# Kernel optimization log

Hardware: AMD Instinct MI355X
Metric: run time of the kernel (lower is better)

Reference implementation:

```python
import jax, jax.numpy as jnp
import numpy as np

H = 100
EPS = 1e-5


def _ln(x, g, b):
    m = jnp.mean(x, axis=-1, keepdims=True)
    v = jnp.mean((x - m) ** 2, axis=-1, keepdims=True)
    return (x - m) / jnp.sqrt(v + EPS) * g + b


def _enc(x, W, b, g, be):
    # Linear -> Tanh -> LayerNorm
    return _ln(jnp.tanh(x @ W + b), g, be)


def setup_inputs() -> dict:
    key = jax.random.key(0)
    ks = jax.random.split(key, 16)
    B, N = 32768, 16
    obs_dim = 4 + 3 * N + 2 * (N - 1) + 2 * N  # 114
    d = {
        'inputs': jax.random.normal(ks[0], (B, obs_dim), dtype=jnp.float32),
        'agent_num': N,
        'sW': jax.random.normal(ks[1], (4, H), dtype=jnp.float32) * 0.5,
        'sb': jnp.zeros((H,), jnp.float32),
        'sg': jnp.ones((H,), jnp.float32),
        'sbe': jnp.zeros((H,), jnp.float32),
        'oW': jax.random.normal(ks[2], (2, H), dtype=jnp.float32) * 0.5,
        'ob': jnp.zeros((H,), jnp.float32),
        'og': jnp.ones((H,), jnp.float32),
        'obe': jnp.zeros((H,), jnp.float32),
        'lW': jax.random.normal(ks[3], (3, H), dtype=jnp.float32) * 0.5,
        'lb': jnp.zeros((H,), jnp.float32),
        'lg': jnp.ones((H,), jnp.float32),
        'lbe': jnp.zeros((H,), jnp.float32),
        'gW': jax.random.normal(ks[4], (2, H), dtype=jnp.float32) * 0.5,
        'gb': jnp.zeros((H,), jnp.float32),
        'gg': jnp.ones((H,), jnp.float32),
        'gbe': jnp.zeros((H,), jnp.float32),
        'Ac': jax.random.normal(ks[5], (H, H), dtype=jnp.float32) * 0.1,
        'Lc': jax.random.normal(ks[6], (H, H), dtype=jnp.float32) * 0.1,
        'fcW': jax.random.normal(ks[7], (H, H), dtype=jnp.float32) * 0.1,
        'fcb': jnp.zeros((H,), jnp.float32),
        'fcg': jnp.ones((H,), jnp.float32),
        'fcbe': jnp.zeros((H,), jnp.float32),
        'f1W': jax.random.normal(ks[8], (4 * H, H), dtype=jnp.float32) * 0.05,
        'f1b': jnp.zeros((H,), jnp.float32),
        'f1g': jnp.ones((H,), jnp.float32),
        'f1be': jnp.zeros((H,), jnp.float32),
        'f2W': jax.random.normal(ks[9], (H, H), dtype=jnp.float32) * 0.1,
        'f2b': jnp.zeros((H,), jnp.float32),
        'f2g': jnp.ones((H,), jnp.float32),
        'f2be': jnp.zeros((H,), jnp.float32),
    }
    return d


def reference(inputs, agent_num, sW, sb, sg, sbe, oW, ob, og, obe, lW, lb, lg, lbe, gW, gb, gg, gbe, Ac, Lc, fcW, fcb, fcg, fcbe, f1W, f1b, f1g, f1be, f2W, f2b, f2g, f2be):
    N = agent_num
    B = inputs.shape[0]
    self_emb = _enc(inputs[:, :4], sW, sb, sg, sbe)  # [B,H]
    lm = inputs[:, 4:4 + 3 * N].reshape(B, N, 3)
    off = 4 + 3 * N
    oth = inputs[:, off:off + 2 * (N - 1)].reshape(B, N - 1, 2)
    off2 = off + 2 * (N - 1)
    gl = inputs[:, off2:off2 + 2 * N].reshape(B, N, 2)
    oth_e = _enc(oth, oW, ob, og, obe)    # [B,N-1,H]
    lm_e = _enc(lm, lW, lb, lg, lbe)      # [B,N,H]
    gl_e = _enc(gl, gW, gb, gg, gbe)      # [B,N,H]
    qa = self_emb @ Ac                    # [B,H]
    ql = self_emb @ Lc                    # [B,H] (also used for goal: bug preserved from source)
    alpha_a = jax.nn.softmax(jnp.einsum('bh,bnh->bn', qa, oth_e), axis=1)
    va = jnp.einsum('bn,bnh->bh', alpha_a, oth_e)
    alpha_l = jax.nn.softmax(jnp.einsum('bh,bnh->bn', ql, lm_e), axis=1)
    vl = jnp.einsum('bn,bnh->bh', alpha_l, lm_e)
    alpha_g = jax.nn.softmax(jnp.einsum('bh,bnh->bn', ql, gl_e), axis=1)
    vg = jnp.einsum('bn,bnh->bh', alpha_g, gl_e)
    gi = _enc(self_emb, fcW, fcb, fcg, fcbe)
    x = jnp.concatenate([gi, va, vl, vg], axis=1)  # [B,4H]
    h = _enc(x, f1W, f1b, f1g, f1be)
    return _enc(h, f2W, f2b, f2g, f2be)
```

## Files before the change

kernel.cpp:

```cpp
#include <hip/hip_runtime.h>
#include <math.h>

#define OBS 114
#define ROWS_PER_BLOCK 16
#define BSTRIDE 104

__device__ __forceinline__ float fast_tanh(float x) {
    float e = __expf(2.0f * x);
    return 1.0f - 2.0f * __builtin_amdgcn_rcpf(e + 1.0f);
}

template<int CTRL>
__device__ __forceinline__ float dpp_add(float x) {
    int y = __builtin_amdgcn_update_dpp(0, __float_as_int(x), CTRL, 0xF, 0xF, true);
    return x + __int_as_float(y);
}
__device__ __forceinline__ float row16_sum(float x) {
    x = dpp_add<0xB1>(x);
    x = dpp_add<0x4E>(x);
    x = dpp_add<0x124>(x);
    x = dpp_add<0x128>(x);
    return x;
}
__device__ __forceinline__ float f4c(const float4& v, int j) {
    return j==0?v.x: j==1?v.y: j==2?v.z: v.w;
}

__global__ __launch_bounds__(256) void repack_kernel(
    const float* __restrict__ Ac, const float* __restrict__ Lc,
    const float* __restrict__ fcW, const float* __restrict__ f1W,
    const float* __restrict__ f2W, float* __restrict__ ws)
{
    int tid = blockIdx.x*256 + threadIdx.x;
    if (tid >= 800*128) return;
    int krow = tid >> 7;
    int idx  = tid & 127;
    int j = idx >> 3, i = idx & 7;
    int h = j + 16*i;
    const float* src; int k;
    if (krow < 100)      { src = Ac;  k = krow; }
    else if (krow < 200) { src = Lc;  k = krow-100; }
    else if (krow < 300) { src = fcW; k = krow-200; }
    else if (krow < 700) { src = f1W; k = krow-300; }
    else                 { src = f2W; k = krow-700; }
    float v = (i < 7 && h < 100) ? src[k*100 + h] : 0.f;
    ws[tid] = v;
}

template<int NK4>
__device__ __forceinline__ void mm16(const float* __restrict__ Wp,
    const float (*sbuf)[BSTRIDE], int R0, int R1, int j, float acc[7][2])
{
    const float* wp = Wp + j*8;
#pragma unroll 2
    for (int k4 = 0; k4 < NK4; ++k4) {
        float4 xa = *(const float4*)&sbuf[R0][k4*4];
        float4 xb = *(const float4*)&sbuf[R1][k4*4];
#pragma unroll
        for (int jj=0;jj<4;++jj) {
            const float* w8 = wp + (size_t)(k4*4+jj)*128;
            float4 wlo = *(const float4*)w8;
            float4 whi = *(const float4*)(w8+4);
            float w[7] = {wlo.x,wlo.y,wlo.z,wlo.w,whi.x,whi.y,whi.z};
            float xka = f4c(xa,jj), xkb = f4c(xb,jj);
#pragma unroll
            for (int i=0;i<7;++i) {
                acc[i][0] = fmaf(xka, w[i], acc[i][0]);
                acc[i][1] = fmaf(xkb, w[i], acc[i][1]);
            }
        }
    }
}

template<int K, int NA>
__device__ __forceinline__ void attn16(
    const float* __restrict__ W, const float* __restrict__ bb,
    const float* __restrict__ gp, const float* __restrict__ bep,
    const float* __restrict__ in, int xoff,
    float (*sbuf)[BSTRIDE],
    int rowAc, int rowBc, int RA, int RB,
    const float qacc[7][2],
    const int hc[7], const float msk[7])
{
    float w[K][7], bias[7], g[7], be[7];
#pragma unroll
    for (int i=0;i<7;++i) {
#pragma unroll
        for (int k=0;k<K;++k) w[k][i] = W[k*100 + hc[i]] * msk[i];
        bias[i] = bb[hc[i]] * msk[i];
        g[i]    = gp[hc[i]] * msk[i];
        be[i]   = bep[hc[i]];
    }
    float qg[2][7], C1[2];
#pragma unroll
    for (int b=0;b<2;++b) {
        float c = 0.f;
#pragma unroll
        for (int i=0;i<7;++i) { qg[b][i] = qacc[i][b]*g[i]; c += qg[b][i]; }
        C1[b] = row16_sum(c);
    }
    const float* xr0 = in + (size_t)rowAc*OBS + xoff;
    const float* xr1 = in + (size_t)rowBc*OBS + xoff;
    float s[2] = {0.f,0.f}, bacc[2] = {0.f,0.f};
    float A[2][7];
#pragma unroll
    for (int b=0;b<2;++b)
#pragma unroll
        for (int i=0;i<7;++i) A[b][i]=0.f;

#pragma unroll 1
    for (int n=0;n<NA;++n) {
        float x0[K], x1[K];
#pragma unroll
        for (int k=0;k<K;++k) { x0[k] = xr0[n*K+k]; x1[k] = xr1[n*K+k]; }
        float t[2][7], sa[2], sq[2], sd[2];
#pragma unroll
        for (int b=0;b<2;++b) { sa[b]=0.f; sq[b]=0.f; sd[b]=0.f; }
#pragma unroll
        for (int i=0;i<7;++i) {
#pragma unroll
            for (int b=0;b<2;++b) {
                float a = bias[i];
#pragma unroll
                for (int k=0;k<K;++k) a = fmaf(b ? x1[k] : x0[k], w[k][i], a);
                float tt = fast_tanh(a);
                t[b][i] = tt;
                sa[b] += tt;
                sq[b] = fmaf(tt,tt,sq[b]);
                sd[b] = fmaf(qg[b][i],tt,sd[b]);
            }
        }
#pragma unroll
        for (int b=0;b<2;++b) { sa[b]=row16_sum(sa[b]); sq[b]=row16_sum(sq[b]); sd[b]=row16_sum(sd[b]); }
#pragma unroll
        for (int b=0;b<2;++b) {
            float mean = sa[b]*0.01f;
            float var  = fmaf(sq[b],0.01f,-mean*mean);
            float rinv = __builtin_amdgcn_rsqf(var + 1e-5f);
            float logit = (sd[b]-mean*C1[b])*rinv;
            float wgt = __expf(fminf(logit,80.f));
            s[b] += wgt;
            float wr = wgt*rinv;
            bacc[b] = fmaf(wr,mean,bacc[b]);
#pragma unroll
            for (int i=0;i<7;++i) A[b][i] = fmaf(wr,t[b][i],A[b][i]);
        }
    }
#pragma unroll
    for (int b=0;b<2;++b) {
        int R = b ? RB : RA;
        float inv = __builtin_amdgcn_rcpf(s[b]);
#pragma unroll
        for (int i=0;i<7;++i)
            if (msk[i]>0.f) sbuf[R][hc[i]] = fmaf(g[i], (A[b][i]-bacc[b])*inv, be[i]);
    }
}

__device__ __forceinline__ void ln_pair(const float acc[7][2],
    const float* __restrict__ bp, const float* __restrict__ gp, const float* __restrict__ bep,
    const int hc[7], const float msk[7], float outv[2][7])
{
    float bias[7], g[7], be[7];
#pragma unroll
    for (int i=0;i<7;++i) { bias[i]=bp[hc[i]]*msk[i]; g[i]=gp[hc[i]]; be[i]=bep[hc[i]]; }
    float t[2][7], sa[2], sq[2];
#pragma unroll
    for (int b=0;b<2;++b) { sa[b]=0.f; sq[b]=0.f; }
#pragma unroll
    for (int i=0;i<7;++i) {
#pragma unroll
        for (int b=0;b<2;++b) {
            float tt = fast_tanh(acc[i][b] + bias[i]);
            t[b][i] = tt; sa[b] += tt*msk[i]; sq[b] = fmaf(tt*msk[i],tt,sq[b]);
        }
    }
#pragma unroll
    for (int b=0;b<2;++b) { sa[b]=row16_sum(sa[b]); sq[b]=row16_sum(sq[b]); }
#pragma unroll
    for (int b=0;b<2;++b) {
        float mean = sa[b]*0.01f;
        float var  = fmaf(sq[b],0.01f,-mean*mean);
        float rinv = __builtin_amdgcn_rsqf(var + 1e-5f);
#pragma unroll
        for (int i=0;i<7;++i) outv[b][i] = fmaf((t[b][i]-mean)*rinv, g[i], be[i]);
    }
}

__global__ __launch_bounds__(128, 4)
void obs_encoder_kernel(const float* __restrict__ in,
    const float* __restrict__ sW, const float* __restrict__ sb, const float* __restrict__ sg, const float* __restrict__ sbe,
    const float* __restrict__ oW, const float* __restrict__ ob, const float* __restrict__ og, const float* __restrict__ obe,
    const float* __restrict__ lW, const float* __restrict__ lb, const float* __restrict__ lg, const float* __restrict__ lbe,
    const float* __restrict__ gW, const float* __restrict__ gb, const float* __restrict__ gg_, const float* __restrict__ gbe,
    const float* __restrict__ fcb, const float* __restrict__ fcg, const float* __restrict__ fcbe,
    const float* __restrict__ f1b, const float* __restrict__ f1g, const float* __restrict__ f1be,
    const float* __restrict__ f2b, const float* __restrict__ f2g, const float* __restrict__ f2be,
    const float* __restrict__ wsf,
    float* __restrict__ out, int B)
{
    const int lane = threadIdx.x & 63;
    const int wv   = threadIdx.x >> 6;
    const int j    = lane & 15;
    const int rw   = lane >> 4;
    const int rowBase = blockIdx.x*ROWS_PER_BLOCK + wv*8;
    const int rowA = rowBase + rw;
    const int rowB = rowBase + 4 + rw;
    const int RA = wv*8 + rw, RB = RA + 4;
    const int rowAc = min(rowA, B-1), rowBc = min(rowB, B-1);

    int hc[7]; float msk[7];
#pragma unroll
    for (int i=0;i<7;++i) {
        int h = j + 16*i;
        bool v = h < 100;
        hc[i] = v ? h : 99;
        msk[i] = v ? 1.f : 0.f;
    }

    __shared__ __align__(16) float sbuf[ROWS_PER_BLOCK][BSTRIDE];

    const float* Acp = wsf;
    const float* Lcp = wsf + 12800;
    const float* fcp = wsf + 25600;
    const float* f1p = wsf + 38400;
    const float* f2p = wsf + 89600;

    {
        float w[4][7], bias[7], g[7], be[7];
#pragma unroll
        for (int i=0;i<7;++i) {
#pragma unroll
            for (int k=0;k<4;++k) w[k][i] = sW[k*100 + hc[i]] * msk[i];
            bias[i] = sb[hc[i]] * msk[i]; g[i] = sg[hc[i]]; be[i] = sbe[hc[i]];
        }
        const float* xr0 = in + (size_t)rowAc*OBS;
        const float* xr1 = in + (size_t)rowBc*OBS;
        float x[2][4];
#pragma unroll
        for (int k=0;k<4;++k) { x[0][k]=xr0[k]; x[1][k]=xr1[k]; }
        float t[2][7], sa[2], sq[2];
#pragma unroll
        for (int b=0;b<2;++b) { sa[b]=0.f; sq[b]=0.f; }
#pragma unroll
        for (int i=0;i<7;++i) {
#pragma unroll
            for (int b=0;b<2;++b) {
                float a = bias[i];
#pragma unroll
                for (int k=0;k<4;++k) a = fmaf(x[b][k], w[k][i], a);
                float tt = fast_tanh(a);
                t[b][i] = tt; sa[b] += tt*msk[i]; sq[b] = fmaf(tt*msk[i],tt,sq[b]);
            }
        }
#pragma unroll
        for (int b=0;b<2;++b) { sa[b]=row16_sum(sa[b]); sq[b]=row16_sum(sq[b]); }
#pragma unroll
        for (int b=0;b<2;++b) {
            int R = b ? RB : RA;
            float mean = sa[b]*0.01f;
            float var  = fmaf(sq[b],0.01f,-mean*mean);
            float rinv = __builtin_amdgcn_rsqf(var + 1e-5f);
#pragma unroll
            for (int i=0;i<7;++i)
                if (msk[i] > 0.f) sbuf[R][hc[i]] = fmaf((t[b][i]-mean)*rinv, g[i], be[i]);
        }
    }

    float accA[7][2], accL[7][2], accF[7][2];
#pragma unroll
    for (int i=0;i<7;++i) { accA[i][0]=accA[i][1]=accL[i][0]=accL[i][1]=accF[i][0]=accF[i][1]=0.f; }
    mm16<25>(Acp, sbuf, RA, RB, j, accA);
    mm16<25>(Lcp, sbuf, RA, RB, j, accL);
    mm16<25>(fcp, sbuf, RA, RB, j, accF);

    float f1a[7][2];
#pragma unroll
    for (int i=0;i<7;++i) { f1a[i][0]=0.f; f1a[i][1]=0.f; }

    {
        float outv[2][7];
        ln_pair(accF, fcb, fcg, fcbe, hc, msk, outv);
#pragma unroll
        for (int b=0;b<2;++b) {
            int R = b ? RB : RA;
#pragma unroll
            for (int i=0;i<7;++i)
                if (msk[i] > 0.f) sbuf[R][hc[i]] = outv[b][i];
        }
    }
    mm16<25>(f1p, sbuf, RA, RB, j, f1a);

    attn16<2,15>(oW, ob, og,  obe, in, 52, sbuf, rowAc, rowBc, RA, RB, accA, hc, msk);
    mm16<25>(f1p + 100*128, sbuf, RA, RB, j, f1a);
    attn16<3,16>(lW, lb, lg,  lbe, in, 4,  sbuf, rowAc, rowBc, RA, RB, accL, hc, msk);
    mm16<25>(f1p + 200*128, sbuf, RA, RB, j, f1a);
    attn16<2,16>(gW, gb, gg_, gbe, in, 82, sbuf, rowAc, rowBc, RA, RB, accL, hc, msk);
    mm16<25>(f1p + 300*128, sbuf, RA, RB, j, f1a);

    {
        float outv[2][7];
        ln_pair(f1a, f1b, f1g, f1be, hc, msk, outv);
#pragma unroll
        for (int b=0;b<2;++b) {
            int R = b ? RB : RA;
#pragma unroll
            for (int i=0;i<7;++i)
                if (msk[i] > 0.f) sbuf[R][hc[i]] = outv[b][i];
        }
    }

    {
        float acc[7][2];
#pragma unroll
        for (int i=0;i<7;++i) { acc[i][0]=0.f; acc[i][1]=0.f; }
        mm16<25>(f2p, sbuf, RA, RB, j, acc);
        float outv[2][7];
        ln_pair(acc, f2b, f2g, f2be, hc, msk, outv);
#pragma unroll
        for (int b=0;b<2;++b) {
            int row = b ? rowB : rowA;
            if (row < B) {
#pragma unroll
                for (int i=0;i<7;++i)
                    if (msk[i] > 0.f)
                        out[(size_t)row*100 + hc[i]] = outv[b][i];
            }
        }
    }
}

extern "C" void kernel_launch(void* const* d_in, const int* in_sizes, int n_in,
                              void* d_out, int out_size, void* d_ws, size_t ws_size,
                              hipStream_t stream) {
    const float* in  = (const float*)d_in[0];
    const float* sW  = (const float*)d_in[2];
    const float* sb  = (const float*)d_in[3];
    const float* sg  = (const float*)d_in[4];
    const float* sbe = (const float*)d_in[5];
    const float* oW  = (const float*)d_in[6];
    const float* ob  = (const float*)d_in[7];
    const float* og  = (const float*)d_in[8];
    const float* obe = (const float*)d_in[9];
    const float* lW  = (const float*)d_in[10];
    const float* lb  = (const float*)d_in[11];
    const float* lg  = (const float*)d_in[12];
    const float* lbe = (const float*)d_in[13];
    const float* gW  = (const float*)d_in[14];
    const float* gb  = (const float*)d_in[15];
    const float* gg  = (const float*)d_in[16];
    const float* gbe = (const float*)d_in[17];
    const float* Ac  = (const float*)d_in[18];
    const float* Lc  = (const float*)d_in[19];
    const float* fcW = (const float*)d_in[20];
    const float* fcb = (const float*)d_in[21];
    const float* fcg = (const float*)d_in[22];
    const float* fcbe= (const float*)d_in[23];
    const float* f1W = (const float*)d_in[24];
    const float* f1b = (const float*)d_in[25];
    const float* f1g = (const float*)d_in[26];
    const float* f1be= (const float*)d_in[27];
    const float* f2W = (const float*)d_in[28];
    const float* f2b = (const float*)d_in[29];
    const float* f2g = (const float*)d_in[30];
    const float* f2be= (const float*)d_in[31];
    float* out = (float*)d_out;
    float* wsf = (float*)d_ws;

    int B = in_sizes[0] / OBS;
    repack_kernel<<<(800*128 + 255)/256, 256, 0, stream>>>(Ac, Lc, fcW, f1W, f2W, wsf);
    int blocks = (B + ROWS_PER_BLOCK - 1) / ROWS_PER_BLOCK;
    obs_encoder_kernel<<<blocks, 128, 0, stream>>>(in,
        sW, sb, sg, sbe, oW, ob, og, obe, lW, lb, lg, lbe, gW, gb, gg, gbe,
        fcb, fcg, fcbe, f1b, f1g, f1be, f2b, f2g, f2be,
        wsf, out, B);
}
```

Baseline: 368.1 us.

## Process one row per thread group instead of two to raise occupancy

Each 16-lane group now handles a single batch row rather than two, halving the per-thread accumulator and attention state. The block grows from 128 to 256 threads, with launch bounds raised to 8 blocks per CU, so the same 16 rows per block are spread over 4 waves. The aim is to cut register pressure and raise occupancy to hide latency better. In exchange, each weight value loaded in the matmuls is reused across half as many rows, which doubles weight-load traffic per row.

New measurement: 568.4 us. 54.4% more time.

```diff
diff --git a/kernel.cpp b/kernel.cpp
--- a/kernel.cpp
+++ b/kernel.cpp
@@ -49,25 +49,21 @@
 
 template<int NK4>
 __device__ __forceinline__ void mm16(const float* __restrict__ Wp,
-    const float (*sbuf)[BSTRIDE], int R0, int R1, int j, float acc[7][2])
+    const float (*sbuf)[BSTRIDE], int R, int j, float acc[7])
 {
     const float* wp = Wp + j*8;
 #pragma unroll 2
     for (int k4 = 0; k4 < NK4; ++k4) {
-        float4 xa = *(const float4*)&sbuf[R0][k4*4];
-        float4 xb = *(const float4*)&sbuf[R1][k4*4];
+        float4 xa = *(const float4*)&sbuf[R][k4*4];
 #pragma unroll
         for (int jj=0;jj<4;++jj) {
             const float* w8 = wp + (size_t)(k4*4+jj)*128;
             float4 wlo = *(const float4*)w8;
             float4 whi = *(const float4*)(w8+4);
             float w[7] = {wlo.x,wlo.y,wlo.z,wlo.w,whi.x,whi.y,whi.z};
-            float xka = f4c(xa,jj), xkb = f4c(xb,jj);
-#pragma unroll
-            for (int i=0;i<7;++i) {
-                acc[i][0] = fmaf(xka, w[i], acc[i][0]);
-                acc[i][1] = fmaf(xkb, w[i], acc[i][1]);
-            }
+            float xk = f4c(xa,jj);
+#pragma unroll
+            for (int i=0;i<7;++i) acc[i] = fmaf(xk, w[i], acc[i]);
         }
     }
 }
@@ -78,8 +74,8 @@
     const float* __restrict__ gp, const float* __restrict__ bep,
     const float* __restrict__ in, int xoff,
     float (*sbuf)[BSTRIDE],
-    int rowAc, int rowBc, int RA, int RB,
-    const float qacc[7][2],
+    int rowc, int R,
+    const float qacc[7],
     const int hc[7], const float msk[7])
 {
     float w[K][7], bias[7], g[7], be[7];
@@ -91,102 +87,72 @@
         g[i]    = gp[hc[i]] * msk[i];
         be[i]   = bep[hc[i]];
     }
-    float qg[2][7], C1[2];
-#pragma unroll
-    for (int b=0;b<2;++b) {
-        float c = 0.f;
-#pragma unroll
-        for (int i=0;i<7;++i) { qg[b][i] = qacc[i][b]*g[i]; c += qg[b][i]; }
-        C1[b] = row16_sum(c);
-    }
-    const float* xr0 = in + (size_t)rowAc*OBS + xoff;
-    const float* xr1 = in + (size_t)rowBc*OBS + xoff;
-    float s[2] = {0.f,0.f}, bacc[2] = {0.f,0.f};
-    float A[2][7];
-#pragma unroll
-    for (int b=0;b<2;++b)
-#pragma unroll
-        for (int i=0;i<7;++i) A[b][i]=0.f;
+    float qg[7];
+    float c = 0.f;
+#pragma unroll
+    for (int i=0;i<7;++i) { qg[i] = qacc[i]*g[i]; c += qg[i]; }
+    float C1 = row16_sum(c);
+
+    const float* xr = in + (size_t)rowc*OBS + xoff;
+    float s = 0.f, bacc = 0.f;
+    float A[7];
+#pragma unroll
+    for (int i=0;i<7;++i) A[i]=0.f;
 
 #pragma unroll 1
     for (int n=0;n<NA;++n) {
-        float x0[K], x1[K];
-#pragma unroll
-        for (int k=0;k<K;++k) { x0[k] = xr0[n*K+k]; x1[k] = xr1[n*K+k]; }
-        float t[2][7], sa[2], sq[2], sd[2];
-#pragma unroll
-        for (int b=0;b<2;++b) { sa[b]=0.f; sq[b]=0.f; sd[b]=0.f; }
+        float x[K];
+#pragma unroll
+        for (int k=0;k<K;++k) x[k] = xr[n*K+k];
+        float t[7], sa=0.f, sq=0.f, sd=0.f;
 #pragma unroll
         for (int i=0;i<7;++i) {
-#pragma unroll
-            for (int b=0;b<2;++b) {
-                float a = bias[i];
-#pragma unroll
-                for (int k=0;k<K;++k) a = fmaf(b ? x1[k] : x0[k], w[k][i], a);
-                float tt = fast_tanh(a);
-                t[b][i] = tt;
-                sa[b] += tt;
-                sq[b] = fmaf(tt,tt,sq[b]);
-                sd[b] = fmaf(qg[b][i],tt,sd[b]);
-            }
-        }
-#pragma unroll
-        for (int b=0;b<2;++b) { sa[b]=row16_sum(sa[b]); sq[b]=row16_sum(sq[b]); sd[b]=row16_sum(sd[b]); }
-#pragma unroll
-        for (int b=0;b<2;++b) {
-            float mean = sa[b]*0.01f;
-            float var  = fmaf(sq[b],0.01f,-mean*mean);
-            float rinv = __builtin_amdgcn_rsqf(var + 1e-5f);
-            float logit = (sd[b]-mean*C1[b])*rinv;
-            float wgt = __expf(fminf(logit,80.f));
-            s[b] += wgt;
-            float wr = wgt*rinv;
-            bacc[b] = fmaf(wr,mean,bacc[b]);
-#pragma unroll
-            for (int i=0;i<7;++i) A[b][i] = fmaf(wr,t[b][i],A[b][i]);
-        }
-    }
-#pragma unroll
-    for (int b=0;b<2;++b) {
-        int R = b ? RB : RA;
-        float inv = __builtin_amdgcn_rcpf(s[b]);
-#pragma unroll
-        for (int i=0;i<7;++i)
-            if (msk[i]>0.f) sbuf[R][hc[i]] = fmaf(g[i], (A[b][i]-bacc[b])*inv, be[i]);
-    }
-}
-
-__device__ __forceinline__ void ln_pair(const float acc[7][2],
+            float a = bias[i];
+#pragma unroll
+            for (int k=0;k<K;++k) a = fmaf(x[k], w[k][i], a);
+            float tt = fast_tanh(a);
+            t[i] = tt;
+            sa += tt;
+            sq = fmaf(tt,tt,sq);
+            sd = fmaf(qg[i],tt,sd);
+        }
+        sa = row16_sum(sa); sq = row16_sum(sq); sd = row16_sum(sd);
+        float mean = sa*0.01f;
+        float var  = fmaf(sq,0.01f,-mean*mean);
+        float rinv = __builtin_amdgcn_rsqf(var + 1e-5f);
+        float logit = (sd-mean*C1)*rinv;
+        float wgt = __expf(fminf(logit,80.f));
+        s += wgt;
+        float wr = wgt*rinv;
+        bacc = fmaf(wr,mean,bacc);
+#pragma unroll
+        for (int i=0;i<7;++i) A[i] = fmaf(wr,t[i],A[i]);
+    }
+    float inv = __builtin_amdgcn_rcpf(s);
+#pragma unroll
+    for (int i=0;i<7;++i)
+        if (msk[i]>0.f) sbuf[R][hc[i]] = fmaf(g[i], (A[i]-bacc)*inv, be[i]);
+}
+
+__device__ __forceinline__ void ln_row(const float acc[7],
     const float* __restrict__ bp, const float* __restrict__ gp, const float* __restrict__ bep,
-    const int hc[7], const float msk[7], float outv[2][7])
-{
-    float bias[7], g[7], be[7];
-#pragma unroll
-    for (int i=0;i<7;++i) { bias[i]=bp[hc[i]]*msk[i]; g[i]=gp[hc[i]]; be[i]=bep[hc[i]]; }
-    float t[2][7], sa[2], sq[2];
-#pragma unroll
-    for (int b=0;b<2;++b) { sa[b]=0.f; sq[b]=0.f; }
+    const int hc[7], const float msk[7], float outv[7])
+{
+    float t[7], sa=0.f, sq=0.f;
 #pragma unroll
     for (int i=0;i<7;++i) {
-#pragma unroll
-        for (int b=0;b<2;++b) {
-            float tt = fast_tanh(acc[i][b] + bias[i]);
-            t[b][i] = tt; sa[b] += tt*msk[i]; sq[b] = fmaf(tt*msk[i],tt,sq[b]);
-        }
-    }
-#pragma unroll
-    for (int b=0;b<2;++b) { sa[b]=row16_sum(sa[b]); sq[b]=row16_sum(sq[b]); }
-#pragma unroll
-    for (int b=0;b<2;++b) {
-        float mean = sa[b]*0.01f;
-        float var  = fmaf(sq[b],0.01f,-mean*mean);
-        float rinv = __builtin_amdgcn_rsqf(var + 1e-5f);
-#pragma unroll
-        for (int i=0;i<7;++i) outv[b][i] = fmaf((t[b][i]-mean)*rinv, g[i], be[i]);
-    }
-}
-
-__global__ __launch_bounds__(128, 4)
+        float tt = fast_tanh(acc[i] + bp[hc[i]]*msk[i]);
+        t[i] = tt; sa += tt*msk[i]; sq = fmaf(tt*msk[i],tt,sq);
+    }
+    sa = row16_sum(sa); sq = row16_sum(sq);
+    float mean = sa*0.01f;
+    float var  = fmaf(sq,0.01f,-mean*mean);
+    float rinv = __builtin_amdgcn_rsqf(var + 1e-5f);
+#pragma unroll
+    for (int i=0;i<7;++i) outv[i] = fmaf((t[i]-mean)*rinv, gp[hc[i]], bep[hc[i]]);
+}
+
+__global__ __launch_bounds__(256, 8)
 void obs_encoder_kernel(const float* __restrict__ in,
     const float* __restrict__ sW, const float* __restrict__ sb, const float* __restrict__ sg, const float* __restrict__ sbe,
     const float* __restrict__ oW, const float* __restrict__ ob, const float* __restrict__ og, const float* __restrict__ obe,
@@ -202,11 +168,9 @@
     const int wv   = threadIdx.x >> 6;
     const int j    = lane & 15;
     const int rw   = lane >> 4;
-    const int rowBase = blockIdx.x*ROWS_PER_BLOCK + wv*8;
-    const int rowA = rowBase + rw;
-    const int rowB = rowBase + 4 + rw;
-    const int RA = wv*8 + rw, RB = RA + 4;
-    const int rowAc = min(rowA, B-1), rowBc = min(rowB, B-1);
+    const int R    = wv*4 + rw;
+    const int row  = blockIdx.x*ROWS_PER_BLOCK + R;
+    const int rowc = min(row, B-1);
 
     int hc[7]; float msk[7];
 #pragma unroll
@@ -233,98 +197,75 @@
             for (int k=0;k<4;++k) w[k][i] = sW[k*100 + hc[i]] * msk[i];
             bias[i] = sb[hc[i]] * msk[i]; g[i] = sg[hc[i]]; be[i] = sbe[hc[i]];
         }
-        const float* xr0 = in + (size_t)rowAc*OBS;
-        const float* xr1 = in + (size_t)rowBc*OBS;
-        float x[2][4];
-#pragma unroll
-        for (int k=0;k<4;++k) { x[0][k]=xr0[k]; x[1][k]=xr1[k]; }
-        float t[2][7], sa[2], sq[2];
-#pragma unroll
-        for (int b=0;b<2;++b) { sa[b]=0.f; sq[b]=0.f; }
+        const float* xr = in + (size_t)rowc*OBS;
+        float x[4];
+#pragma unroll
+        for (int k=0;k<4;++k) x[k] = xr[k];
+        float t[7], sa=0.f, sq=0.f;
 #pragma unroll
         for (int i=0;i<7;++i) {
-#pragma unroll
-            for (int b=0;b<2;++b) {
-                float a = bias[i];
-#pragma unroll
-                for (int k=0;k<4;++k) a = fmaf(x[b][k], w[k][i], a);
-                float tt = fast_tanh(a);
-                t[b][i] = tt; sa[b] += tt*msk[i]; sq[b] = fmaf(tt*msk[i],tt,sq[b]);
-            }
-        }
-#pragma unroll
-        for (int b=0;b<2;++b) { sa[b]=row16_sum(sa[b]); sq[b]=row16_sum(sq[b]); }
-#pragma unroll
-        for (int b=0;b<2;++b) {
-            int R = b ? RB : RA;
-            float mean = sa[b]*0.01f;
-            float var  = fmaf(sq[b],0.01f,-mean*mean);
-            float rinv = __builtin_amdgcn_rsqf(var + 1e-5f);
+            float a = bias[i];
+#pragma unroll
+            for (int k=0;k<4;++k) a = fmaf(x[k], w[k][i], a);
+            float tt = fast_tanh(a);
+            t[i] = tt; sa += tt*msk[i]; sq = fmaf(tt*msk[i],tt,sq);
+        }
+        sa = row16_sum(sa); sq = row16_sum(sq);
+        float mean = sa*0.01f;
+        float var  = fmaf(sq,0.01f,-mean*mean);
+        float rinv = __builtin_amdgcn_rsqf(var + 1e-5f);
+#pragma unroll
+        for (int i=0;i<7;++i)
+            if (msk[i] > 0.f) sbuf[R][hc[i]] = fmaf((t[i]-mean)*rinv, g[i], be[i]);
+    }
+
+    float accA[7], accL[7], accF[7];
+#pragma unroll
+    for (int i=0;i<7;++i) { accA[i]=0.f; accL[i]=0.f; accF[i]=0.f; }
+    mm16<25>(Acp, sbuf, R, j, accA);
+    mm16<25>(Lcp, sbuf, R, j, accL);
+    mm16<25>(fcp, sbuf, R, j, accF);
+
+    float f1a[7];
+#pragma unroll
+    for (int i=0;i<7;++i) f1a[i]=0.f;
+
+    {
+        float outv[7];
+        ln_row(accF, fcb, fcg, fcbe, hc, msk, outv);
+#pragma unroll
+        for (int i=0;i<7;++i)
+            if (msk[i] > 0.f) sbuf[R][hc[i]] = outv[i];
+    }
+    mm16<25>(f1p, sbuf, R, j, f1a);
+
+    attn16<2,15>(oW, ob, og,  obe, in, 52, sbuf, rowc, R, accA, hc, msk);
+    mm16<25>(f1p + 100*128, sbuf, R, j, f1a);
+    attn16<3,16>(lW, lb, lg,  lbe, in, 4,  sbuf, rowc, R, accL, hc, msk);
+    mm16<25>(f1p + 200*128, sbuf, R, j, f1a);
+    attn16<2,16>(gW, gb, gg_, gbe, in, 82, sbuf, rowc, R, accL, hc, msk);
+    mm16<25>(f1p + 300*128, sbuf, R, j, f1a);
+
+    {
+        float outv[7];
+        ln_row(f1a, f1b, f1g, f1be, hc, msk, outv);
+#pragma unroll
+        for (int i=0;i<7;++i)
+            if (msk[i] > 0.f) sbuf[R][hc[i]] = outv[i];
+    }
+
+    {
+        float acc[7];
+#pragma unroll
+        for (int i=0;i<7;++i) acc[i]=0.f;
+        mm16<25>(f2p, sbuf, R, j, acc);
+        float outv[7];
+        ln_row(acc, f2b, f2g, f2be, hc, msk, outv);
+        if (row < B) {
 #pragma unroll
             for (int i=0;i<7;++i)
-                if (msk[i] > 0.f) sbuf[R][hc[i]] = fmaf((t[b][i]-mean)*rinv, g[i], be[i]);
-        }
-    }
-
-    float accA[7][2], accL[7][2], accF[7][2];
-#pragma unroll
-    for (int i=0;i<7;++i) { accA[i][0]=accA[i][1]=accL[i][0]=accL[i][1]=accF[i][0]=accF[i][1]=0.f; }
-    mm16<25>(Acp, sbuf, RA, RB, j, accA);
-    mm16<25>(Lcp, sbuf, RA, RB, j, accL);
-    mm16<25>(fcp, sbuf, RA, RB, j, accF);
-
-    float f1a[7][2];
-#pragma unroll
-    for (int i=0;i<7;++i) { f1a[i][0]=0.f; f1a[i][1]=0.f; }
-
-    {
-        float outv[2][7];
-        ln_pair(accF, fcb, fcg, fcbe, hc, msk, outv);
-#pragma unroll
-        for (int b=0;b<2;++b) {
-            int R = b ? RB : RA;
-#pragma unroll
-            for (int i=0;i<7;++i)
-                if (msk[i] > 0.f) sbuf[R][hc[i]] = outv[b][i];
-        }
-    }
-    mm16<25>(f1p, sbuf, RA, RB, j, f1a);
-
-    attn16<2,15>(oW, ob, og,  obe, in, 52, sbuf, rowAc, rowBc, RA, RB, accA, hc, msk);
-    mm16<25>(f1p + 100*128, sbuf, RA, RB, j, f1a);
-    attn16<3,16>(lW, lb, lg,  lbe, in, 4,  sbuf, rowAc, rowBc, RA, RB, accL, hc, msk);
-    mm16<25>(f1p + 200*128, sbuf, RA, RB, j, f1a);
-    attn16<2,16>(gW, gb, gg_, gbe, in, 82, sbuf, rowAc, rowBc, RA, RB, accL, hc, msk);
-    mm16<25>(f1p + 300*128, sbuf, RA, RB, j, f1a);
-
-    {
-        float outv[2][7];
-        ln_pair(f1a, f1b, f1g, f1be, hc, msk, outv);
-#pragma unroll
-        for (int b=0;b<2;++b) {
-            int R = b ? RB : RA;
-#pragma unroll
-            for (int i=0;i<7;++i)
-                if (msk[i] > 0.f) sbuf[R][hc[i]] = outv[b][i];
-        }
-    }
-
-    {
-        float acc[7][2];
-#pragma unroll
-        for (int i=0;i<7;++i) { acc[i][0]=0.f; acc[i][1]=0.f; }
-        mm16<25>(f2p, sbuf, RA, RB, j, acc);
-        float outv[2][7];
-        ln_pair(acc, f2b, f2g, f2be, hc, msk, outv);
-#pragma unroll
-        for (int b=0;b<2;++b) {
-            int row = b ? rowB : rowA;
-            if (row < B) {
-#pragma unroll
-                for (int i=0;i<7;++i)
-                    if (msk[i] > 0.f)
-                        out[(size_t)row*100 + hc[i]] = outv[b][i];
-            }
+                if (msk[i] > 0.f)
+                    out[(size_t)row*100 + hc[i]] = outv[i];
         }
     }
 }
@@ -369,7 +310,7 @@
     int B = in_sizes[0] / OBS;
     repack_kernel<<<(800*128 + 255)/256, 256, 0, stream>>>(Ac, Lc, fcW, f1W, f2W, wsf);
     int blocks = (B + ROWS_PER_BLOCK - 1) / ROWS_PER_BLOCK;
-    obs_encoder_kernel<<<blocks, 128, 0, stream>>>(in,
+    obs_encoder_kernel<<<blocks, 256, 0, stream>>>(in,
         sW, sb, sg, sbe, oW, ob, og, obe, lW, lb, lg, lbe, gW, gb, gg, gbe,
         fcb, fcg, fcbe, f1b, f1g, f1be, f2b, f2g, f2be,
         wsf, out, B);
```

## Process four rows per thread with single-wave blocks for more weight reuse

Applied to the files above, without the earlier changes.

Each 16-lane group now handles four consecutive batch rows instead of two, so every weight float4 loaded in the matmul loops feeds four FMAs rather than two. Blocks shrink to one 64-thread wave covering the same 16 rows, and launch bounds change to (64,2). This halves weight traffic per row and removes a wave of per-block overhead. In exchange it roughly doubles accumulator register pressure (several 7x4 arrays live across stages), which can cut occupancy or cause spills, and the attention stages carry more live state per lane.

Result: faster. 311.4 us (-15.4%).

```diff
diff --git a/kernel.cpp b/kernel.cpp
--- a/kernel.cpp
+++ b/kernel.cpp
@@ -49,24 +49,28 @@
 
 template<int NK4>
 __device__ __forceinline__ void mm16(const float* __restrict__ Wp,
-    const float (*sbuf)[BSTRIDE], int R0, int R1, int j, float acc[7][2])
+    const float (*sbuf)[BSTRIDE], int R0, int j, float acc[7][4])
 {
     const float* wp = Wp + j*8;
 #pragma unroll 2
     for (int k4 = 0; k4 < NK4; ++k4) {
-        float4 xa = *(const float4*)&sbuf[R0][k4*4];
-        float4 xb = *(const float4*)&sbuf[R1][k4*4];
+        float4 x0 = *(const float4*)&sbuf[R0+0][k4*4];
+        float4 x1 = *(const float4*)&sbuf[R0+1][k4*4];
+        float4 x2 = *(const float4*)&sbuf[R0+2][k4*4];
+        float4 x3 = *(const float4*)&sbuf[R0+3][k4*4];
 #pragma unroll
         for (int jj=0;jj<4;++jj) {
             const float* w8 = wp + (size_t)(k4*4+jj)*128;
             float4 wlo = *(const float4*)w8;
             float4 whi = *(const float4*)(w8+4);
             float w[7] = {wlo.x,wlo.y,wlo.z,wlo.w,whi.x,whi.y,whi.z};
-            float xka = f4c(xa,jj), xkb = f4c(xb,jj);
+            float xk0 = f4c(x0,jj), xk1 = f4c(x1,jj), xk2 = f4c(x2,jj), xk3 = f4c(x3,jj);
 #pragma unroll
             for (int i=0;i<7;++i) {
-                acc[i][0] = fmaf(xka, w[i], acc[i][0]);
-                acc[i][1] = fmaf(xkb, w[i], acc[i][1]);
+                acc[i][0] = fmaf(xk0, w[i], acc[i][0]);
+                acc[i][1] = fmaf(xk1, w[i], acc[i][1]);
+                acc[i][2] = fmaf(xk2, w[i], acc[i][2]);
+                acc[i][3] = fmaf(xk3, w[i], acc[i][3]);
             }
         }
     }
@@ -78,8 +82,8 @@
     const float* __restrict__ gp, const float* __restrict__ bep,
     const float* __restrict__ in, int xoff,
     float (*sbuf)[BSTRIDE],
-    int rowAc, int rowBc, int RA, int RB,
-    const float qacc[7][2],
+    int base, int R0, int B,
+    const float qacc[7][4],
     const int hc[7], const float msk[7])
 {
     float w[K][7], bias[7], g[7], be[7];
@@ -91,38 +95,44 @@
         g[i]    = gp[hc[i]] * msk[i];
         be[i]   = bep[hc[i]];
     }
-    float qg[2][7], C1[2];
-#pragma unroll
-    for (int b=0;b<2;++b) {
+    float qg[4][7], C1[4];
+#pragma unroll
+    for (int b=0;b<4;++b) {
         float c = 0.f;
 #pragma unroll
         for (int i=0;i<7;++i) { qg[b][i] = qacc[i][b]*g[i]; c += qg[b][i]; }
         C1[b] = row16_sum(c);
     }
-    const float* xr0 = in + (size_t)rowAc*OBS + xoff;
-    const float* xr1 = in + (size_t)rowBc*OBS + xoff;
-    float s[2] = {0.f,0.f}, bacc[2] = {0.f,0.f};
-    float A[2][7];
-#pragma unroll
-    for (int b=0;b<2;++b)
+    const float* xr[4];
+#pragma unroll
+    for (int b=0;b<4;++b)
+        xr[b] = in + (size_t)min(base + R0 + b, B-1)*OBS + xoff;
+
+    float s[4], bacc[4], A[4][7];
+#pragma unroll
+    for (int b=0;b<4;++b) {
+        s[b]=0.f; bacc[b]=0.f;
 #pragma unroll
         for (int i=0;i<7;++i) A[b][i]=0.f;
+    }
 
 #pragma unroll 1
     for (int n=0;n<NA;++n) {
-        float x0[K], x1[K];
-#pragma unroll
-        for (int k=0;k<K;++k) { x0[k] = xr0[n*K+k]; x1[k] = xr1[n*K+k]; }
-        float t[2][7], sa[2], sq[2], sd[2];
-#pragma unroll
-        for (int b=0;b<2;++b) { sa[b]=0.f; sq[b]=0.f; sd[b]=0.f; }
+        float x[4][K];
+#pragma unroll
+        for (int b=0;b<4;++b)
+#pragma unroll
+            for (int k=0;k<K;++k) x[b][k] = xr[b][n*K+k];
+        float t[4][7], sa[4], sq[4], sd[4];
+#pragma unroll
+        for (int b=0;b<4;++b) { sa[b]=0.f; sq[b]=0.f; sd[b]=0.f; }
 #pragma unroll
         for (int i=0;i<7;++i) {
 #pragma unroll
-            for (int b=0;b<2;++b) {
+            for (int b=0;b<4;++b) {
                 float a = bias[i];
 #pragma unroll
-                for (int k=0;k<K;++k) a = fmaf(b ? x1[k] : x0[k], w[k][i], a);
+                for (int k=0;k<K;++k) a = fmaf(x[b][k], w[k][i], a);
                 float tt = fast_tanh(a);
                 t[b][i] = tt;
                 sa[b] += tt;
@@ -131,9 +141,9 @@
             }
         }
 #pragma unroll
-        for (int b=0;b<2;++b) { sa[b]=row16_sum(sa[b]); sq[b]=row16_sum(sq[b]); sd[b]=row16_sum(sd[b]); }
-#pragma unroll
-        for (int b=0;b<2;++b) {
+        for (int b=0;b<4;++b) { sa[b]=row16_sum(sa[b]); sq[b]=row16_sum(sq[b]); sd[b]=row16_sum(sd[b]); }
+#pragma unroll
+        for (int b=0;b<4;++b) {
             float mean = sa[b]*0.01f;
             float var  = fmaf(sq[b],0.01f,-mean*mean);
             float rinv = __builtin_amdgcn_rsqf(var + 1e-5f);
@@ -147,46 +157,45 @@
         }
     }
 #pragma unroll
-    for (int b=0;b<2;++b) {
-        int R = b ? RB : RA;
+    for (int b=0;b<4;++b) {
         float inv = __builtin_amdgcn_rcpf(s[b]);
 #pragma unroll
         for (int i=0;i<7;++i)
-            if (msk[i]>0.f) sbuf[R][hc[i]] = fmaf(g[i], (A[b][i]-bacc[b])*inv, be[i]);
-    }
-}
-
-__device__ __forceinline__ void ln_pair(const float acc[7][2],
+            if (msk[i]>0.f) sbuf[R0+b][hc[i]] = fmaf(g[i], (A[b][i]-bacc[b])*inv, be[i]);
+    }
+}
+
+__device__ __forceinline__ void ln_quad(const float acc[7][4],
     const float* __restrict__ bp, const float* __restrict__ gp, const float* __restrict__ bep,
-    const int hc[7], const float msk[7], float outv[2][7])
-{
-    float bias[7], g[7], be[7];
-#pragma unroll
-    for (int i=0;i<7;++i) { bias[i]=bp[hc[i]]*msk[i]; g[i]=gp[hc[i]]; be[i]=bep[hc[i]]; }
-    float t[2][7], sa[2], sq[2];
-#pragma unroll
-    for (int b=0;b<2;++b) { sa[b]=0.f; sq[b]=0.f; }
+    const int hc[7], const float msk[7], float outv[4][7])
+{
+    float bias[7], ga[7], be[7];
+#pragma unroll
+    for (int i=0;i<7;++i) { bias[i]=bp[hc[i]]*msk[i]; ga[i]=gp[hc[i]]; be[i]=bep[hc[i]]; }
+    float t[4][7], sa[4], sq[4];
+#pragma unroll
+    for (int b=0;b<4;++b) { sa[b]=0.f; sq[b]=0.f; }
 #pragma unroll
     for (int i=0;i<7;++i) {
 #pragma unroll
-        for (int b=0;b<2;++b) {
+        for (int b=0;b<4;++b) {
             float tt = fast_tanh(acc[i][b] + bias[i]);
             t[b][i] = tt; sa[b] += tt*msk[i]; sq[b] = fmaf(tt*msk[i],tt,sq[b]);
         }
     }
 #pragma unroll
-    for (int b=0;b<2;++b) { sa[b]=row16_sum(sa[b]); sq[b]=row16_sum(sq[b]); }
-#pragma unroll
-    for (int b=0;b<2;++b) {
+    for (int b=0;b<4;++b) { sa[b]=row16_sum(sa[b]); sq[b]=row16_sum(sq[b]); }
+#pragma unroll
+    for (int b=0;b<4;++b) {
         float mean = sa[b]*0.01f;
         float var  = fmaf(sq[b],0.01f,-mean*mean);
         float rinv = __builtin_amdgcn_rsqf(var + 1e-5f);
 #pragma unroll
-        for (int i=0;i<7;++i) outv[b][i] = fmaf((t[b][i]-mean)*rinv, g[i], be[i]);
-    }
-}
-
-__global__ __launch_bounds__(128, 4)
+        for (int i=0;i<7;++i) outv[b][i] = fmaf((t[b][i]-mean)*rinv, ga[i], be[i]);
+    }
+}
+
+__global__ __launch_bounds__(64, 2)
 void obs_encoder_kernel(const float* __restrict__ in,
     const float* __restrict__ sW, const float* __restrict__ sb, const float* __restrict__ sg, const float* __restrict__ sbe,
     const float* __restrict__ oW, const float* __restrict__ ob, const float* __restrict__ og, const float* __restrict__ obe,
@@ -198,15 +207,11 @@
     const float* __restrict__ wsf,
     float* __restrict__ out, int B)
 {
-    const int lane = threadIdx.x & 63;
-    const int wv   = threadIdx.x >> 6;
+    const int lane = threadIdx.x;
     const int j    = lane & 15;
-    const int rw   = lane >> 4;
-    const int rowBase = blockIdx.x*ROWS_PER_BLOCK + wv*8;
-    const int rowA = rowBase + rw;
-    const int rowB = rowBase + 4 + rw;
-    const int RA = wv*8 + rw, RB = RA + 4;
-    const int rowAc = min(rowA, B-1), rowBc = min(rowB, B-1);
+    const int grp  = lane >> 4;
+    const int R0   = grp*4;
+    const int base = blockIdx.x*ROWS_PER_BLOCK;
 
     int hc[7]; float msk[7];
 #pragma unroll
@@ -233,18 +238,20 @@
             for (int k=0;k<4;++k) w[k][i] = sW[k*100 + hc[i]] * msk[i];
             bias[i] = sb[hc[i]] * msk[i]; g[i] = sg[hc[i]]; be[i] = sbe[hc[i]];
         }
-        const float* xr0 = in + (size_t)rowAc*OBS;
-        const float* xr1 = in + (size_t)rowBc*OBS;
-        float x[2][4];
-#pragma unroll
-        for (int k=0;k<4;++k) { x[0][k]=xr0[k]; x[1][k]=xr1[k]; }
-        float t[2][7], sa[2], sq[2];
-#pragma unroll
-        for (int b=0;b<2;++b) { sa[b]=0.f; sq[b]=0.f; }
+        float x[4][4];
+#pragma unroll
+        for (int b=0;b<4;++b) {
+            const float* xr = in + (size_t)min(base + R0 + b, B-1)*OBS;
+#pragma unroll
+            for (int k=0;k<4;++k) x[b][k] = xr[k];
+        }
+        float t[4][7], sa[4], sq[4];
+#pragma unroll
+        for (int b=0;b<4;++b) { sa[b]=0.f; sq[b]=0.f; }
 #pragma unroll
         for (int i=0;i<7;++i) {
 #pragma unroll
-            for (int b=0;b<2;++b) {
+            for (int b=0;b<4;++b) {
                 float a = bias[i];
 #pragma unroll
                 for (int k=0;k<4;++k) a = fmaf(x[b][k], w[k][i], a);
@@ -253,72 +260,73 @@
             }
         }
 #pragma unroll
-        for (int b=0;b<2;++b) { sa[b]=row16_sum(sa[b]); sq[b]=row16_sum(sq[b]); }
-#pragma unroll
-        for (int b=0;b<2;++b) {
-            int R = b ? RB : RA;
+        for (int b=0;b<4;++b) { sa[b]=row16_sum(sa[b]); sq[b]=row16_sum(sq[b]); }
+#pragma unroll
+        for (int b=0;b<4;++b) {
             float mean = sa[b]*0.01f;
             float var  = fmaf(sq[b],0.01f,-mean*mean);
             float rinv = __builtin_amdgcn_rsqf(var + 1e-5f);
 #pragma unroll
             for (int i=0;i<7;++i)
-                if (msk[i] > 0.f) sbuf[R][hc[i]] = fmaf((t[b][i]-mean)*rinv, g[i], be[i]);
-        }
-    }
-
-    float accA[7][2], accL[7][2], accF[7][2];
-#pragma unroll
-    for (int i=0;i<7;++i) { accA[i][0]=accA[i][1]=accL[i][0]=accL[i][1]=accF[i][0]=accF[i][1]=0.f; }
-    mm16<25>(Acp, sbuf, RA, RB, j, accA);
-    mm16<25>(Lcp, sbuf, RA, RB, j, accL);
-    mm16<25>(fcp, sbuf, RA, RB, j, accF);
-
-    float f1a[7][2];
-#pragma unroll
-    for (int i=0;i<7;++i) { f1a[i][0]=0.f; f1a[i][1]=0.f; }
+                if (msk[i] > 0.f) sbuf[R0+b][hc[i]] = fmaf((t[b][i]-mean)*rinv, g[i], be[i]);
+        }
+    }
+
+    float accA[7][4], accL[7][4], accF[7][4];
+#pragma unroll
+    for (int i=0;i<7;++i)
+#pragma unroll
+        for (int b=0;b<4;++b) { accA[i][b]=0.f; accL[i][b]=0.f; accF[i][b]=0.f; }
+    mm16<25>(Acp, sbuf, R0, j, accA);
+    mm16<25>(Lcp, sbuf, R0, j, accL);
+    mm16<25>(fcp, sbuf, R0, j, accF);
+
+    float f1a[7][4];
+#pragma unroll
+    for (int i=0;i<7;++i)
+#pragma unroll
+        for (int b=0;b<4;++b) f1a[i][b]=0.f;
 
     {
-        float outv[2][7];
-        ln_pair(accF, fcb, fcg, fcbe, hc, msk, outv);
-#pragma unroll
-        for (int b=0;b<2;++b) {
-            int R = b ? RB : RA;
+        float outv[4][7];
+        ln_quad(accF, fcb, fcg, fcbe, hc, msk, outv);
+#pragma unroll
+        for (int b=0;b<4;++b)
 #pragma unroll
             for (int i=0;i<7;++i)
-                if (msk[i] > 0.f) sbuf[R][hc[i]] = outv[b][i];
-        }
-    }
-    mm16<25>(f1p, sbuf, RA, RB, j, f1a);
-
-    attn16<2,15>(oW, ob, og,  obe, in, 52, sbuf, rowAc, rowBc, RA, RB, accA, hc, msk);
-    mm16<25>(f1p + 100*128, sbuf, RA, RB, j, f1a);
-    attn16<3,16>(lW, lb, lg,  lbe, in, 4,  sbuf, rowAc, rowBc, RA, RB, accL, hc, msk);
-    mm16<25>(f1p + 200*128, sbuf, RA, RB, j, f1a);
-    attn16<2,16>(gW, gb, gg_, gbe, in, 82, sbuf, rowAc, rowBc, RA, RB, accL, hc, msk);
-    mm16<25>(f1p + 300*128, sbuf, RA, RB, j, f1a);
+                if (msk[i] > 0.f) sbuf[R0+b][hc[i]] = outv[b][i];
+    }
+    mm16<25>(f1p, sbuf, R0, j, f1a);
+
+    attn16<2,15>(oW, ob, og,  obe, in, 52, sbuf, base, R0, B, accA, hc, msk);
+    mm16<25>(f1p + 100*128, sbuf, R0, j, f1a);
+    attn16<3,16>(lW, lb, lg,  lbe, in, 4,  sbuf, base, R0, B, accL, hc, msk);
+    mm16<25>(f1p + 200*128, sbuf, R0, j, f1a);
+    attn16<2,16>(gW, gb, gg_, gbe, in, 82, sbuf, base, R0, B, accL, hc, msk);
+    mm16<25>(f1p + 300*128, sbuf, R0, j, f1a);
 
     {
-        float outv[2][7];
-        ln_pair(f1a, f1b, f1g, f1be, hc, msk, outv);
-#pragma unroll
-        for (int b=0;b<2;++b) {
-            int R = b ? RB : RA;
+        float outv[4][7];
+        ln_quad(f1a, f1b, f1g, f1be, hc, msk, outv);
+#pragma unroll
+        for (int b=0;b<4;++b)
 #pragma unroll
             for (int i=0;i<7;++i)
-                if (msk[i] > 0.f) sbuf[R][hc[i]] = outv[b][i];
-        }
+                if (msk[i] > 0.f) sbuf[R0+b][hc[i]] = outv[b][i];
     }
 
     {
-        float acc[7][2];
-#pragma unroll
-        for (int i=0;i<7;++i) { acc[i][0]=0.f; acc[i][1]=0.f; }
-        mm16<25>(f2p, sbuf, RA, RB, j, acc);
-        float outv[2][7];
-        ln_pair(acc, f2b, f2g, f2be, hc, msk, outv);
-#pragma unroll
-        for (int b=0;b<2;++b) {
-            int row = b ? rowB : rowA;
+        float acc[7][4];
+#pragma unroll
+        for (int i=0;i<7;++i)
+#pragma unroll
+            for (int b=0;b<4;++b) acc[i][b]=0.f;
+        mm16<25>(f2p, sbuf, R0, j, acc);
+        float outv[4][7];
+        ln_quad(acc, f2b, f2g, f2be, hc, msk, outv);
+#pragma unroll
+        for (int b=0;b<4;++b) {
+            int row = base + R0 + b;
             if (row < B) {
 #pragma unroll
                 for (int i=0;i<7;++i)
@@ -369,7 +377,7 @@
     int B = in_sizes[0] / OBS;
     repack_kernel<<<(800*128 + 255)/256, 256, 0, stream>>>(Ac, Lc, fcW, f1W, f2W, wsf);
     int blocks = (B + ROWS_PER_BLOCK - 1) / ROWS_PER_BLOCK;
-    obs_encoder_kernel<<<blocks, 128, 0, stream>>>(in,
+    obs_encoder_kernel<<<blocks, 64, 0, stream>>>(in,
         sW, sb, sg, sbe, oW, ob, og, obe, lW, lb, lg, lbe, gW, gb, gg, gbe,
         fcb, fcg, fcbe, f1b, f1g, f1be, f2b, f2g, f2be,
         wsf, out, B);
```
